# Kernel optimization log

Hardware: AMD Instinct MI355X
Metric: run time of the kernel (lower is better)

## Reference

```python
import jax, jax.numpy as jnp
import numpy as np

B, T, D, C = 16, 1500, 768, 1024

def setup_inputs() -> dict:
    key = jax.random.key(0)
    k1, k2 = jax.random.split(key)
    embed = jax.random.normal(k1, (B, T, D), dtype=jnp.float32)
    cluster_centers = jax.random.normal(k2, (C, D), dtype=jnp.float32)
    return {"embed": embed, "cluster_centers": cluster_centers}

def reference(embed, cluster_centers):
    # Faithful to: dists = -torch.cdist(embed, centers, p=2); clusters = dists.argmax(-1)
    # Euclidean distance via ||e||^2 - 2 e.c + ||c||^2 (GEMM-friendly form).
    e_sq = jnp.sum(embed * embed, axis=-1, keepdims=True)            # (b, t, 1)
    c_sq = jnp.sum(cluster_centers * cluster_centers, axis=-1)       # (c,)
    cross = jnp.einsum('btd,cd->btc', embed, cluster_centers)        # (b, t, c)
    d2 = jnp.maximum(e_sq - 2.0 * cross + c_sq, 0.0)
    dists = -jnp.sqrt(d2)                                            # negative L2 distance
    clusters = jnp.argmax(dists, axis=-1)                            # (b, t) int
    return clusters
```

## Files before the change

### kernel.cpp

```cpp
#include <hip/hip_runtime.h>
#include <cstdint>
#include <cstddef>

#define MROWS 24000
#define NCOLS 1024
#define KDIM  768
#define MT 188
#define KT 48
#define NT 4

typedef _Float16 f16x8  __attribute__((ext_vector_type(8)));
typedef float    f32x16 __attribute__((ext_vector_type(16)));

typedef __attribute__((address_space(1))) void as1_void;
typedef __attribute__((address_space(3))) void as3_void;

#define A_BYTES   (188ull*48*8192)
#define B_OFF     A_BYTES
#define B_BYTES   (4ull*48*16384)
#define CH_OFF    (A_BYTES + B_BYTES)
#define PART_OFF  (CH_OFF + 4096)
#define WS_NEED   (PART_OFF + 24064ull*4*8)

__global__ void k_tile_A(const float* __restrict__ E, _Float16* __restrict__ Aw) {
  int bid = blockIdx.x;
  int mt = bid / 48, kt = bid % 48;
  int t = threadIdx.x;
  int r = t >> 1, p = t & 1;
  int row = mt * 128 + r;
  __shared__ _Float16 lh[2][128][8];
  __shared__ _Float16 ll[2][128][8];
  float x[8];
  if (row < MROWS) {
    const float4* s4 = (const float4*)(E + (size_t)row * KDIM + kt * 16 + p * 8);
    float4 v0 = s4[0], v1 = s4[1];
    x[0]=v0.x; x[1]=v0.y; x[2]=v0.z; x[3]=v0.w; x[4]=v1.x; x[5]=v1.y; x[6]=v1.z; x[7]=v1.w;
  } else {
#pragma unroll
    for (int e = 0; e < 8; ++e) x[e] = 0.f;
  }
#pragma unroll
  for (int e = 0; e < 8; ++e) {
    _Float16 h = (_Float16)x[e];
    lh[p][r][e] = h;
    ll[p][r][e] = (_Float16)(x[e] - (float)h);
  }
  __syncthreads();
  const uint4* sh = (const uint4*)&lh[0][0][0];
  const uint4* sl = (const uint4*)&ll[0][0][0];
  uint4* dst = (uint4*)(Aw + (size_t)bid * 4096);
  dst[t]       = sh[t];
  dst[256 + t] = sl[t];
}

__global__ void k_tile_B(const float* __restrict__ C, _Float16* __restrict__ Bw) {
  int bid = blockIdx.x;
  int nt = bid / 48, kt = bid % 48;
  int t = threadIdx.x;
  int c = t >> 1, p = t & 1;
  __shared__ _Float16 lh[2][256][8];
  __shared__ _Float16 ll[2][256][8];
  const float4* s4 = (const float4*)(C + (size_t)(nt * 256 + c) * KDIM + kt * 16 + p * 8);
  float4 v0 = s4[0], v1 = s4[1];
  float x[8] = {v0.x, v0.y, v0.z, v0.w, v1.x, v1.y, v1.z, v1.w};
#pragma unroll
  for (int e = 0; e < 8; ++e) {
    _Float16 h = (_Float16)x[e];
    lh[p][c][e] = h;
    ll[p][c][e] = (_Float16)(x[e] - (float)h);
  }
  __syncthreads();
  const uint4* sh = (const uint4*)&lh[0][0][0];
  const uint4* sl = (const uint4*)&ll[0][0][0];
  uint4* dst = (uint4*)(Bw + (size_t)bid * 8192);
  dst[t]       = sh[t];
  dst[512 + t] = sl[t];
}

__global__ void k_chalf(const float* __restrict__ C, float* __restrict__ ch) {
  int c = blockIdx.x, t = threadIdx.x;
  const float* src = C + (size_t)c * KDIM;
  float sq = 0.f;
#pragma unroll
  for (int i = 0; i < 3; ++i) {
    float x = src[t + i * 256];
    sq = fmaf(x, x, sq);
  }
#pragma unroll
  for (int m = 1; m < 64; m <<= 1) sq += __shfl_xor(sq, m, 64);
  __shared__ float part[4];
  if ((t & 63) == 0) part[t >> 6] = sq;
  __syncthreads();
  if (t == 0) ch[c] = 0.5f * ((part[0] + part[1]) + (part[2] + part[3]));
}

__global__ __launch_bounds__(512, 4) void k_gemm(
    const _Float16* __restrict__ Aw, const _Float16* __restrict__ Bw,
    const float* __restrict__ ch, uint2* __restrict__ part) {
  __shared__ __align__(16) char smem[2][24576];
  __shared__ float red_v[4][128];
  __shared__ int   red_i[4][128];

  int bid0 = blockIdx.x;
  int swz = (bid0 & 7) * 94 + (bid0 >> 3);
  int nt = swz / MT, mt = swz % MT;

  const int tid = threadIdx.x, lane = tid & 63, wid = tid >> 6;
  const int wm = wid >> 2, wn = wid & 3;
  const int lo5 = lane & 31, p = lane >> 5;

  const char* Ab = (const char*)Aw + (size_t)mt * (48 * 8192);
  const char* Bb = (const char*)Bw + (size_t)nt * (48 * 16384);

  auto stage = [&](int buf, int kt) {
    char* sb = smem[buf];
    const char* ga = Ab + kt * 8192;
    const char* gb = Bb + kt * 16384;
    __builtin_amdgcn_global_load_lds((as1_void*)(ga + tid * 16),        (as3_void*)(sb + tid * 16),         16, 0, 0);
    __builtin_amdgcn_global_load_lds((as1_void*)(gb + tid * 16),        (as3_void*)(sb + 8192 + tid * 16),  16, 0, 0);
    __builtin_amdgcn_global_load_lds((as1_void*)(gb + 8192 + tid * 16), (as3_void*)(sb + 16384 + tid * 16), 16, 0, 0);
  };

  f32x16 acc[2][2] = {};

  stage(0, 0);
  __syncthreads();

  int buf = 0;
  for (int kt = 0; kt < KT; ++kt) {
    if (kt + 1 < KT) stage(buf ^ 1, kt + 1);

    const char* sb = smem[buf];
    f16x8 ah[2], al[2], bh[2], bl[2];
#pragma unroll
    for (int mi = 0; mi < 2; ++mi) {
      int off = p * 2048 + (wm * 64 + mi * 32 + lo5) * 16;
      ah[mi] = *(const f16x8*)(sb + off);
      al[mi] = *(const f16x8*)(sb + 4096 + off);
    }
#pragma unroll
    for (int ni = 0; ni < 2; ++ni) {
      int off = p * 4096 + (wn * 64 + ni * 32 + lo5) * 16;
      bh[ni] = *(const f16x8*)(sb + 8192 + off);
      bl[ni] = *(const f16x8*)(sb + 16384 + off);
    }
#pragma unroll
    for (int mi = 0; mi < 2; ++mi)
#pragma unroll
      for (int ni = 0; ni < 2; ++ni) {
        acc[mi][ni] = __builtin_amdgcn_mfma_f32_32x32x16_f16(ah[mi], bh[ni], acc[mi][ni], 0, 0, 0);
        acc[mi][ni] = __builtin_amdgcn_mfma_f32_32x32x16_f16(ah[mi], bl[ni], acc[mi][ni], 0, 0, 0);
        acc[mi][ni] = __builtin_amdgcn_mfma_f32_32x32x16_f16(al[mi], bh[ni], acc[mi][ni], 0, 0, 0);
      }
    __syncthreads();
    buf ^= 1;
  }

  int c0 = nt * 256 + wn * 64 + lo5;
  int c1 = c0 + 32;
  float ch0 = ch[c0];
  float ch1 = ch[c1];
#pragma unroll
  for (int mi = 0; mi < 2; ++mi)
#pragma unroll
    for (int q = 0; q < 16; ++q) {
      float s0 = acc[mi][0][q] - ch0;
      float s1 = acc[mi][1][q] - ch1;
      float v = s0; int ix = c0;
      if (s1 > v) { v = s1; ix = c1; }
#pragma unroll
      for (int m = 1; m <= 16; m <<= 1) {
        float ov = __shfl_xor(v, m, 64);
        int   oi = __shfl_xor(ix, m, 64);
        if (ov > v || (ov == v && oi < ix)) { v = ov; ix = oi; }
      }
      if (lo5 == 0) {
        int rr = (q & 3) + ((q >> 2) << 3) + (p << 2);
        int rloc = wm * 64 + mi * 32 + rr;
        red_v[wn][rloc] = v;
        red_i[wn][rloc] = ix;
      }
    }
  __syncthreads();
  if (tid < 128) {
    float v = red_v[0][tid];
    int ix = red_i[0][tid];
#pragma unroll
    for (int w = 1; w < 4; ++w) {
      float ov = red_v[w][tid];
      int oi = red_i[w][tid];
      if (ov > v) { v = ov; ix = oi; }
    }
    int rowg = mt * 128 + tid;
    part[rowg * 4 + nt] = uint2{ __float_as_uint(v), (unsigned)ix };
  }
}

__global__ void k_merge(const uint2* __restrict__ part, int* __restrict__ out) {
  int r = blockIdx.x * 256 + threadIdx.x;
  if (r >= MROWS) return;
  uint2 b0 = part[r * 4];
  float bvv = __uint_as_float(b0.x);
  int bii = (int)b0.y;
#pragma unroll
  for (int j = 1; j < 4; ++j) {
    uint2 pj = part[r * 4 + j];
    float v = __uint_as_float(pj.x);
    if (v > bvv) { bvv = v; bii = (int)pj.y; }
  }
  out[r] = bii;
}

__global__ void k_naive(const float* __restrict__ E, const float* __restrict__ C,
                        int* __restrict__ out) {
  int row = blockIdx.x * 4 + (threadIdx.x >> 6);
  int lane = threadIdx.x & 63;
  const float* e = E + (size_t)row * KDIM;
  float bvv = -3.4e38f;
  int bii = 0;
  for (int c = 0; c < NCOLS; ++c) {
    const float* cc = C + (size_t)c * KDIM;
    float dot = 0.f, csq = 0.f;
    for (int d = lane; d < KDIM; d += 64) {
      float cv = cc[d];
      dot = fmaf(e[d], cv, dot);
      csq = fmaf(cv, cv, csq);
    }
#pragma unroll
    for (int m = 1; m < 64; m <<= 1) {
      dot += __shfl_xor(dot, m, 64);
      csq += __shfl_xor(csq, m, 64);
    }
    float s = dot - 0.5f * csq;
    if (s > bvv) { bvv = s; bii = c; }
  }
  if (lane == 0) out[row] = bii;
}

extern "C" void kernel_launch(void* const* d_in, const int* in_sizes, int n_in,
                              void* d_out, int out_size, void* d_ws, size_t ws_size,
                              hipStream_t stream) {
  const float* embed   = (const float*)d_in[0];
  const float* centers = (const float*)d_in[1];
  int* out = (int*)d_out;

  if (ws_size >= WS_NEED) {
    char* w = (char*)d_ws;
    _Float16* Aw = (_Float16*)w;
    _Float16* Bw = (_Float16*)(w + B_OFF);
    float*    ch = (float*)(w + CH_OFF);
    uint2*  partb = (uint2*)(w + PART_OFF);
    k_tile_A<<<188 * 48, 256, 0, stream>>>(embed, Aw);
    k_tile_B<<<4 * 48, 512, 0, stream>>>(centers, Bw);
    k_chalf<<<1024, 256, 0, stream>>>(centers, ch);
    k_gemm<<<752, 512, 0, stream>>>(Aw, Bw, ch, partb);
    k_merge<<<94, 256, 0, stream>>>(partb, out);
  } else {
    k_naive<<<6000, 256, 0, stream>>>(embed, centers, out);
  }
}
```

Baseline: 179.3 us.

## Triple-buffer GEMM with 4-wave blocks, larger warp tiles and split staging

Reworks the split-fp16 GEMM to use 256-thread blocks with each wave computing a 64x128 tile instead of 64x64. This raises MFMA work per LDS fragment load and halves the cross-wave argmax reduction. It also moves from double to triple LDS buffering, issuing the next-next tile's loads in two halves between MFMA groups. A counted vmcnt wait plus raw s_barrier replaces __syncthreads, and s_setprio is raised around the MFMA bursts. The costs are more accumulator registers, fewer waves per block for hiding latency, and a hand-written wait count that must match the loads actually in flight.

```diff
diff --git a/kernel.cpp b/kernel.cpp
--- a/kernel.cpp
+++ b/kernel.cpp
@@ -94,80 +94,113 @@
   if (t == 0) ch[c] = 0.5f * ((part[0] + part[1]) + (part[2] + part[3]));
 }
 
-__global__ __launch_bounds__(512, 4) void k_gemm(
+__global__ __launch_bounds__(256, 2) void k_gemm(
     const _Float16* __restrict__ Aw, const _Float16* __restrict__ Bw,
     const float* __restrict__ ch, uint2* __restrict__ part) {
-  __shared__ __align__(16) char smem[2][24576];
-  __shared__ float red_v[4][128];
-  __shared__ int   red_i[4][128];
-
-  int bid0 = blockIdx.x;
-  int swz = (bid0 & 7) * 94 + (bid0 >> 3);
-  int nt = swz / MT, mt = swz % MT;
+  __shared__ __align__(16) char smem[3][24576];
+  __shared__ float red_v[2][128];
+  __shared__ int   red_i[2][128];
+
+  const int bid0 = blockIdx.x;
+  const int swz = (bid0 & 7) * 94 + (bid0 >> 3);
+  const int nt = swz / MT, mt = swz % MT;
 
   const int tid = threadIdx.x, lane = tid & 63, wid = tid >> 6;
-  const int wm = wid >> 2, wn = wid & 3;
+  const int wm = wid >> 1, wn = wid & 1;
   const int lo5 = lane & 31, p = lane >> 5;
 
   const char* Ab = (const char*)Aw + (size_t)mt * (48 * 8192);
   const char* Bb = (const char*)Bw + (size_t)nt * (48 * 16384);
 
-  auto stage = [&](int buf, int kt) {
-    char* sb = smem[buf];
+  auto stage = [&](char* sb, int kt, int half) {
     const char* ga = Ab + kt * 8192;
     const char* gb = Bb + kt * 16384;
-    __builtin_amdgcn_global_load_lds((as1_void*)(ga + tid * 16),        (as3_void*)(sb + tid * 16),         16, 0, 0);
-    __builtin_amdgcn_global_load_lds((as1_void*)(gb + tid * 16),        (as3_void*)(sb + 8192 + tid * 16),  16, 0, 0);
-    __builtin_amdgcn_global_load_lds((as1_void*)(gb + 8192 + tid * 16), (as3_void*)(sb + 16384 + tid * 16), 16, 0, 0);
+    if (half == 0) {
+      __builtin_amdgcn_global_load_lds((as1_void*)(ga + tid * 16),        (as3_void*)(sb + tid * 16),         16, 0, 0);
+      __builtin_amdgcn_global_load_lds((as1_void*)(ga + 4096 + tid * 16), (as3_void*)(sb + 4096 + tid * 16),  16, 0, 0);
+      __builtin_amdgcn_global_load_lds((as1_void*)(gb + tid * 16),        (as3_void*)(sb + 8192 + tid * 16),  16, 0, 0);
+    } else {
+      __builtin_amdgcn_global_load_lds((as1_void*)(gb + 4096 + tid * 16),  (as3_void*)(sb + 12288 + tid * 16), 16, 0, 0);
+      __builtin_amdgcn_global_load_lds((as1_void*)(gb + 8192 + tid * 16),  (as3_void*)(sb + 16384 + tid * 16), 16, 0, 0);
+      __builtin_amdgcn_global_load_lds((as1_void*)(gb + 12288 + tid * 16), (as3_void*)(sb + 20480 + tid * 16), 16, 0, 0);
+    }
   };
 
-  f32x16 acc[2][2] = {};
-
-  stage(0, 0);
-  __syncthreads();
-
-  int buf = 0;
-  for (int kt = 0; kt < KT; ++kt) {
-    if (kt + 1 < KT) stage(buf ^ 1, kt + 1);
-
-    const char* sb = smem[buf];
-    f16x8 ah[2], al[2], bh[2], bl[2];
-#pragma unroll
-    for (int mi = 0; mi < 2; ++mi) {
-      int off = p * 2048 + (wm * 64 + mi * 32 + lo5) * 16;
-      ah[mi] = *(const f16x8*)(sb + off);
-      al[mi] = *(const f16x8*)(sb + 4096 + off);
-    }
-#pragma unroll
-    for (int ni = 0; ni < 2; ++ni) {
-      int off = p * 4096 + (wn * 64 + ni * 32 + lo5) * 16;
-      bh[ni] = *(const f16x8*)(sb + 8192 + off);
-      bl[ni] = *(const f16x8*)(sb + 16384 + off);
-    }
+  f32x16 acc[2][4] = {};
+
+  const int offA0 = p * 2048 + (wm * 64 + lo5) * 16;
+  const int offB0 = p * 4096 + (wn * 128 + lo5) * 16;
+
+  auto ktile = [&](const char* rb, char* wb, int jstage) {
+    f16x8 a[2][2], b[2][2];
 #pragma unroll
     for (int mi = 0; mi < 2; ++mi)
 #pragma unroll
-      for (int ni = 0; ni < 2; ++ni) {
-        acc[mi][ni] = __builtin_amdgcn_mfma_f32_32x32x16_f16(ah[mi], bh[ni], acc[mi][ni], 0, 0, 0);
-        acc[mi][ni] = __builtin_amdgcn_mfma_f32_32x32x16_f16(ah[mi], bl[ni], acc[mi][ni], 0, 0, 0);
-        acc[mi][ni] = __builtin_amdgcn_mfma_f32_32x32x16_f16(al[mi], bh[ni], acc[mi][ni], 0, 0, 0);
-      }
-    __syncthreads();
-    buf ^= 1;
-  }
-
-  int c0 = nt * 256 + wn * 64 + lo5;
-  int c1 = c0 + 32;
-  float ch0 = ch[c0];
-  float ch1 = ch[c1];
+      for (int pl = 0; pl < 2; ++pl)
+        a[mi][pl] = *(const f16x8*)(rb + pl * 4096 + offA0 + mi * 512);
+#pragma unroll
+    for (int ni = 0; ni < 2; ++ni)
+#pragma unroll
+      for (int pl = 0; pl < 2; ++pl)
+        b[ni][pl] = *(const f16x8*)(rb + 8192 + pl * 8192 + offB0 + ni * 512);
+    if (jstage < KT) stage(wb, jstage, 0);
+    __builtin_amdgcn_s_setprio(1);
+#pragma unroll
+    for (int ni = 0; ni < 2; ++ni)
+#pragma unroll
+      for (int mi = 0; mi < 2; ++mi) {
+        acc[mi][ni] = __builtin_amdgcn_mfma_f32_32x32x16_f16(a[mi][0], b[ni][0], acc[mi][ni], 0, 0, 0);
+        acc[mi][ni] = __builtin_amdgcn_mfma_f32_32x32x16_f16(a[mi][0], b[ni][1], acc[mi][ni], 0, 0, 0);
+        acc[mi][ni] = __builtin_amdgcn_mfma_f32_32x32x16_f16(a[mi][1], b[ni][0], acc[mi][ni], 0, 0, 0);
+      }
+    __builtin_amdgcn_s_setprio(0);
+#pragma unroll
+    for (int ni = 0; ni < 2; ++ni)
+#pragma unroll
+      for (int pl = 0; pl < 2; ++pl)
+        b[ni][pl] = *(const f16x8*)(rb + 8192 + pl * 8192 + offB0 + (ni + 2) * 512);
+    if (jstage < KT) stage(wb, jstage, 1);
+    __builtin_amdgcn_s_setprio(1);
+#pragma unroll
+    for (int ni = 0; ni < 2; ++ni)
+#pragma unroll
+      for (int mi = 0; mi < 2; ++mi) {
+        acc[mi][ni + 2] = __builtin_amdgcn_mfma_f32_32x32x16_f16(a[mi][0], b[ni][0], acc[mi][ni + 2], 0, 0, 0);
+        acc[mi][ni + 2] = __builtin_amdgcn_mfma_f32_32x32x16_f16(a[mi][0], b[ni][1], acc[mi][ni + 2], 0, 0, 0);
+        acc[mi][ni + 2] = __builtin_amdgcn_mfma_f32_32x32x16_f16(a[mi][1], b[ni][0], acc[mi][ni + 2], 0, 0, 0);
+      }
+    __builtin_amdgcn_s_setprio(0);
+  };
+
+  auto kbar = [&](bool counted) {
+    if (counted) asm volatile("s_waitcnt vmcnt(6)\n\ts_barrier" ::: "memory");
+    else         asm volatile("s_waitcnt vmcnt(0)\n\ts_barrier" ::: "memory");
+  };
+
+  stage(smem[0], 0, 0); stage(smem[0], 0, 1);
+  stage(smem[1], 1, 0); stage(smem[1], 1, 1);
+
+  for (int j = 0; j < KT; j += 3) {
+    kbar(j + 1 < KT); ktile(smem[0], smem[2], j + 2);
+    kbar(j + 2 < KT); ktile(smem[1], smem[0], j + 3);
+    kbar(j + 3 < KT); ktile(smem[2], smem[1], j + 4);
+  }
+
+  float chv[4];
+#pragma unroll
+  for (int ni = 0; ni < 4; ++ni) chv[ni] = ch[nt * 256 + wn * 128 + ni * 32 + lo5];
+
 #pragma unroll
   for (int mi = 0; mi < 2; ++mi)
 #pragma unroll
     for (int q = 0; q < 16; ++q) {
-      float s0 = acc[mi][0][q] - ch0;
-      float s1 = acc[mi][1][q] - ch1;
-      float v = s0; int ix = c0;
-      if (s1 > v) { v = s1; ix = c1; }
+      float v = acc[mi][0][q] - chv[0];
+      int ix = nt * 256 + wn * 128 + lo5;
+#pragma unroll
+      for (int ni = 1; ni < 4; ++ni) {
+        float s = acc[mi][ni][q] - chv[ni];
+        if (s > v) { v = s; ix = nt * 256 + wn * 128 + ni * 32 + lo5; }
+      }
 #pragma unroll
       for (int m = 1; m <= 16; m <<= 1) {
         float ov = __shfl_xor(v, m, 64);
@@ -185,12 +218,8 @@
   if (tid < 128) {
     float v = red_v[0][tid];
     int ix = red_i[0][tid];
-#pragma unroll
-    for (int w = 1; w < 4; ++w) {
-      float ov = red_v[w][tid];
-      int oi = red_i[w][tid];
-      if (ov > v) { v = ov; ix = oi; }
-    }
+    float ov = red_v[1][tid];
+    if (ov > v) { v = ov; ix = red_i[1][tid]; }
     int rowg = mt * 128 + tid;
     part[rowg * 4 + nt] = uint2{ __float_as_uint(v), (unsigned)ix };
   }
@@ -253,7 +282,7 @@
     k_tile_A<<<188 * 48, 256, 0, stream>>>(embed, Aw);
     k_tile_B<<<4 * 48, 512, 0, stream>>>(centers, Bw);
     k_chalf<<<1024, 256, 0, stream>>>(centers, ch);
-    k_gemm<<<752, 512, 0, stream>>>(Aw, Bw, ch, partb);
+    k_gemm<<<752, 256, 0, stream>>>(Aw, Bw, ch, partb);
     k_merge<<<94, 256, 0, stream>>>(partb, out);
   } else {
     k_naive<<<6000, 256, 0, stream>>>(embed, centers, out);
```

Measured after the change: 178.2 us. About the same (-0.6%).

## Triple-buffer GEMM k-loop with prefetch distance two and interleaved load/MFMA phases

Applied to the files above, without the earlier changes.

The GEMM main loop moves from a double-buffered global-to-LDS pipeline to a rotating triple buffer. Loads are issued two k-tiles ahead, and an explicit s_waitcnt vmcnt replaces the full __syncthreads wait. Each iteration is split into two MFMA phases, with the next-next tile's A/B0 and B1 loads interleaved between them. s_setprio raises wave priority around the MFMA bursts, so the aim is to hide global load latency behind matrix math. In exchange, LDS use per block grows by half and there are more barriers per iteration, which may limit how many blocks fit on each CU.

```diff
diff --git a/kernel.cpp b/kernel.cpp
--- a/kernel.cpp
+++ b/kernel.cpp
@@ -94,16 +94,18 @@
   if (t == 0) ch[c] = 0.5f * ((part[0] + part[1]) + (part[2] + part[3]));
 }
 
+#define MFMA16(a, b, c) __builtin_amdgcn_mfma_f32_32x32x16_f16((a), (b), (c), 0, 0, 0)
+
 __global__ __launch_bounds__(512, 4) void k_gemm(
     const _Float16* __restrict__ Aw, const _Float16* __restrict__ Bw,
     const float* __restrict__ ch, uint2* __restrict__ part) {
-  __shared__ __align__(16) char smem[2][24576];
+  __shared__ __align__(16) char smem[3][24576];
   __shared__ float red_v[4][128];
   __shared__ int   red_i[4][128];
 
-  int bid0 = blockIdx.x;
-  int swz = (bid0 & 7) * 94 + (bid0 >> 3);
-  int nt = swz / MT, mt = swz % MT;
+  const int bid0 = blockIdx.x;
+  const int swz = (bid0 & 7) * 94 + (bid0 >> 3);
+  const int nt = swz / MT, mt = swz % MT;
 
   const int tid = threadIdx.x, lane = tid & 63, wid = tid >> 6;
   const int wm = wid >> 2, wn = wid & 3;
@@ -112,48 +114,67 @@
   const char* Ab = (const char*)Aw + (size_t)mt * (48 * 8192);
   const char* Bb = (const char*)Bw + (size_t)nt * (48 * 16384);
 
-  auto stage = [&](int buf, int kt) {
-    char* sb = smem[buf];
-    const char* ga = Ab + kt * 8192;
-    const char* gb = Bb + kt * 16384;
-    __builtin_amdgcn_global_load_lds((as1_void*)(ga + tid * 16),        (as3_void*)(sb + tid * 16),         16, 0, 0);
-    __builtin_amdgcn_global_load_lds((as1_void*)(gb + tid * 16),        (as3_void*)(sb + 8192 + tid * 16),  16, 0, 0);
-    __builtin_amdgcn_global_load_lds((as1_void*)(gb + 8192 + tid * 16), (as3_void*)(sb + 16384 + tid * 16), 16, 0, 0);
+  auto stageA = [&](char* sb, int kt) {
+    __builtin_amdgcn_global_load_lds((as1_void*)(Ab + kt * 8192 + tid * 16),
+                                     (as3_void*)(sb + tid * 16), 16, 0, 0);
   };
+  auto stageB0 = [&](char* sb, int kt) {
+    __builtin_amdgcn_global_load_lds((as1_void*)(Bb + kt * 16384 + tid * 16),
+                                     (as3_void*)(sb + 8192 + tid * 16), 16, 0, 0);
+  };
+  auto stageB1 = [&](char* sb, int kt) {
+    __builtin_amdgcn_global_load_lds((as1_void*)(Bb + kt * 16384 + 8192 + tid * 16),
+                                     (as3_void*)(sb + 16384 + tid * 16), 16, 0, 0);
+  };
 
   f32x16 acc[2][2] = {};
-
-  stage(0, 0);
-  __syncthreads();
-
-  int buf = 0;
-  for (int kt = 0; kt < KT; ++kt) {
-    if (kt + 1 < KT) stage(buf ^ 1, kt + 1);
-
-    const char* sb = smem[buf];
-    f16x8 ah[2], al[2], bh[2], bl[2];
-#pragma unroll
-    for (int mi = 0; mi < 2; ++mi) {
-      int off = p * 2048 + (wm * 64 + mi * 32 + lo5) * 16;
-      ah[mi] = *(const f16x8*)(sb + off);
-      al[mi] = *(const f16x8*)(sb + 4096 + off);
-    }
-#pragma unroll
-    for (int ni = 0; ni < 2; ++ni) {
-      int off = p * 4096 + (wn * 64 + ni * 32 + lo5) * 16;
-      bh[ni] = *(const f16x8*)(sb + 8192 + off);
-      bl[ni] = *(const f16x8*)(sb + 16384 + off);
-    }
-#pragma unroll
-    for (int mi = 0; mi < 2; ++mi)
-#pragma unroll
-      for (int ni = 0; ni < 2; ++ni) {
-        acc[mi][ni] = __builtin_amdgcn_mfma_f32_32x32x16_f16(ah[mi], bh[ni], acc[mi][ni], 0, 0, 0);
-        acc[mi][ni] = __builtin_amdgcn_mfma_f32_32x32x16_f16(ah[mi], bl[ni], acc[mi][ni], 0, 0, 0);
-        acc[mi][ni] = __builtin_amdgcn_mfma_f32_32x32x16_f16(al[mi], bh[ni], acc[mi][ni], 0, 0, 0);
-      }
-    __syncthreads();
-    buf ^= 1;
+  const int offA = p * 2048 + (wm * 64 + lo5) * 16;
+  const int offB = p * 4096 + (wn * 64 + lo5) * 16;
+
+  char* rb = smem[0];
+  char* nb = smem[1];
+  char* wb = smem[2];
+
+  stageA(smem[0], 0); stageB0(smem[0], 0); stageB1(smem[0], 0);
+  stageA(smem[1], 1); stageB0(smem[1], 1); stageB1(smem[1], 1);
+
+  for (int j = 0; j < KT; ++j) {
+    if (j < KT - 1) asm volatile("s_waitcnt vmcnt(3)" ::: "memory");
+    else            asm volatile("s_waitcnt vmcnt(0)" ::: "memory");
+    __builtin_amdgcn_s_barrier();
+
+    f16x8 ah0 = *(const f16x8*)(rb + offA);
+    f16x8 ah1 = *(const f16x8*)(rb + offA + 512);
+    f16x8 al0 = *(const f16x8*)(rb + 4096 + offA);
+    f16x8 al1 = *(const f16x8*)(rb + 4096 + offA + 512);
+    f16x8 bh0 = *(const f16x8*)(rb + 8192 + offB);
+    f16x8 bl0 = *(const f16x8*)(rb + 16384 + offB);
+    if (j + 2 < KT) { stageA(wb, j + 2); stageB0(wb, j + 2); }
+    __builtin_amdgcn_s_barrier();
+    __builtin_amdgcn_s_setprio(1);
+    acc[0][0] = MFMA16(ah0, bh0, acc[0][0]);
+    acc[0][0] = MFMA16(ah0, bl0, acc[0][0]);
+    acc[0][0] = MFMA16(al0, bh0, acc[0][0]);
+    acc[1][0] = MFMA16(ah1, bh0, acc[1][0]);
+    acc[1][0] = MFMA16(ah1, bl0, acc[1][0]);
+    acc[1][0] = MFMA16(al1, bh0, acc[1][0]);
+    __builtin_amdgcn_s_setprio(0);
+    __builtin_amdgcn_s_barrier();
+
+    f16x8 bh1 = *(const f16x8*)(rb + 8192 + offB + 512);
+    f16x8 bl1 = *(const f16x8*)(rb + 16384 + offB + 512);
+    if (j + 2 < KT) stageB1(wb, j + 2);
+    __builtin_amdgcn_s_barrier();
+    __builtin_amdgcn_s_setprio(1);
+    acc[0][1] = MFMA16(ah0, bh1, acc[0][1]);
+    acc[0][1] = MFMA16(ah0, bl1, acc[0][1]);
+    acc[0][1] = MFMA16(al0, bh1, acc[0][1]);
+    acc[1][1] = MFMA16(ah1, bh1, acc[1][1]);
+    acc[1][1] = MFMA16(ah1, bl1, acc[1][1]);
+    acc[1][1] = MFMA16(al1, bh1, acc[1][1]);
+    __builtin_amdgcn_s_setprio(0);
+
+    char* t = rb; rb = nb; nb = wb; wb = t;
   }
 
   int c0 = nt * 256 + wn * 64 + lo5;
```

Result: faster. 171.0 us (median of 2 runs) (-4.6%).
